# Optimization experiments

Hardware: AMD Instinct MI355X
Metric: run time of the kernel (lower is better)

The kernel has to match this reference:

```python
import jax, jax.numpy as jnp
import numpy as np

N_NODES = 100000   # n_users + n_items
N_EDGES = 1000000  # avg degree ~10
D = 64             # embed_dim
N_LAYERS = 3


def setup_inputs() -> dict:
    key = jax.random.key(0)
    k1, k2, k3, k4 = jax.random.split(key, 4)
    embedding = jax.random.normal(k1, (N_NODES, D), dtype=jnp.float32)
    src = jax.random.randint(k2, (N_EDGES,), 0, N_NODES)
    dst = jax.random.randint(k3, (N_EDGES,), 0, N_NODES)
    # sqrt_degree is a per-node [N,1] positive scale (1/sqrt(deg) in practice)
    sqrt_degree = jax.random.uniform(k4, (N_NODES, 1), dtype=jnp.float32,
                                     minval=0.01, maxval=1.0)
    return {"embedding": embedding, "sqrt_degree": sqrt_degree,
            "src": src, "dst": dst, "n_layers": N_LAYERS}


def reference(embedding, sqrt_degree, src, dst, n_layers):
    n_nodes = embedding.shape[0]
    h = embedding
    acc = embedding  # ego embedding (layer 0)
    for _ in range(n_layers):
        # Aggregator: scale, copy_src gather, segment-sum scatter, scale
        msg = (h * sqrt_degree)[src]                                   # [E, D]
        h = jax.ops.segment_sum(msg, dst, num_segments=n_nodes)        # [N, D]
        h = h * sqrt_degree
        acc = acc + h
    # torch.mean(torch.stack(all_embed, -1), -1)
    return acc / jnp.asarray(n_layers + 1, dtype=embedding.dtype)
```

## Files before the change

### kernel.cpp

```cpp
#include <hip/hip_runtime.h>
#include <hip/hip_fp16.h>


#define N_NODES 100000
#define D 64
#define ND4 (N_NODES * D / 4)
#define SCAN_B 1024
#define NTILES ((N_NODES + SCAN_B - 1) / SCAN_B)
#define NSLICE 8
#define SLICE_DIV 12500
#define D_MASK 0x1FFFF

typedef float        f4v __attribute__((ext_vector_type(4)));
typedef unsigned int u4v __attribute__((ext_vector_type(4)));

union H4 { uint2 u; __half2 h[2]; };
union H8 { u4v u; __half2 h[4]; };

__global__ void init_hist_kernel(const float4* __restrict__ emb,
                                 const float* __restrict__ deg,
                                 const int* __restrict__ dst,
                                 uint2* __restrict__ hs,
                                 int* __restrict__ cnt,
                                 unsigned int* __restrict__ key,
                                 int n4, int nedges) {
    int i = blockIdx.x * blockDim.x + threadIdx.x;
    if (i < nedges) {
        int d = dst[i];
        int r = atomicAdd(&cnt[d], 1);
        key[i] = (unsigned int)d | ((unsigned int)r << 17);
    }
    if (i >= n4) return;
    float dg = deg[i >> 4];
    float4 v = emb[i];
    H4 x;
    x.h[0] = __float22half2_rn(make_float2(v.x * dg, v.y * dg));
    x.h[1] = __float22half2_rn(make_float2(v.z * dg, v.w * dg));
    hs[i] = x.u;
}

__global__ void scanA_kernel(const int* __restrict__ cnt, int* __restrict__ off,
                             int* __restrict__ tsum, int n) {
    __shared__ int sm[SCAN_B];
    int t = threadIdx.x;
    int i = blockIdx.x * SCAN_B + t;
    int x = (i < n) ? cnt[i] : 0;
    sm[t] = x;
    __syncthreads();
    for (int o = 1; o < SCAN_B; o <<= 1) {
        int v = (t >= o) ? sm[t - o] : 0;
        __syncthreads();
        sm[t] += v;
        __syncthreads();
    }
    if (i < n) off[i] = sm[t] - x;
    if (t == SCAN_B - 1) tsum[blockIdx.x] = sm[t];
}

__global__ void scanB_kernel(int* __restrict__ tsum, int ntiles) {
    __shared__ int sm[SCAN_B];
    int t = threadIdx.x;
    int x = (t < ntiles) ? tsum[t] : 0;
    sm[t] = x;
    __syncthreads();
    for (int o = 1; o < SCAN_B; o <<= 1) {
        int v = (t >= o) ? sm[t - o] : 0;
        __syncthreads();
        sm[t] += v;
        __syncthreads();
    }
    if (t < ntiles) tsum[t] = sm[t] - x;
}

__global__ void scanC_kernel(int* __restrict__ off, const int* __restrict__ tsum,
                             int n, int nedges) {
    int i = blockIdx.x * blockDim.x + threadIdx.x;
    if (i >= n) return;
    off[i] += tsum[i >> 10];
    if (i == 0) off[n] = nedges;
}

__global__ void reorder_kernel(const int* __restrict__ src,
                               const unsigned int* __restrict__ key,
                               const int* __restrict__ off,
                               int* __restrict__ ssrc, int nedges) {
    int slice = blockIdx.x & (NSLICE - 1);
    int e = (blockIdx.x >> 3) * blockDim.x + threadIdx.x;
    if (e >= nedges) return;
    unsigned int k = __builtin_nontemporal_load(&key[e]);
    int d = (int)(k & D_MASK);
    if (d / SLICE_DIV != slice) return;
    int r = (int)(k >> 17);
    int p = off[d] + r;
    ssrc[p] = __builtin_nontemporal_load(&src[e]);
}

__device__ __forceinline__ void acc_h8(float* s, u4v u) {
    H8 x; x.u = u;
    #pragma unroll
    for (int k = 0; k < 4; ++k) {
        float2 f = __half22float2(x.h[k]);
        s[2 * k]     += f.x;
        s[2 * k + 1] += f.y;
    }
}

__global__ void aggregate_kernel(const u4v* __restrict__ hs_in,
                                 const int* __restrict__ off,
                                 const int* __restrict__ ssrc,
                                 const float* __restrict__ deg,
                                 const f4v* __restrict__ acc_in,
                                 f4v* __restrict__ acc_out,
                                 u4v* __restrict__ hs_out,
                                 int write_hs, float scale) {
    int tid = blockIdx.x * blockDim.x + threadIdx.x;
    int n = tid >> 3;
    if (n >= N_NODES) return;
    int d8 = tid & 7;
    int start = off[n];
    int end = off[n + 1];
    float s[8] = {0.f, 0.f, 0.f, 0.f, 0.f, 0.f, 0.f, 0.f};

    int j = start;
    for (; j + 8 <= end; j += 8) {
        int i0 = __builtin_nontemporal_load(&ssrc[j]);
        int i1 = __builtin_nontemporal_load(&ssrc[j + 1]);
        int i2 = __builtin_nontemporal_load(&ssrc[j + 2]);
        int i3 = __builtin_nontemporal_load(&ssrc[j + 3]);
        int i4 = __builtin_nontemporal_load(&ssrc[j + 4]);
        int i5 = __builtin_nontemporal_load(&ssrc[j + 5]);
        int i6 = __builtin_nontemporal_load(&ssrc[j + 6]);
        int i7 = __builtin_nontemporal_load(&ssrc[j + 7]);
        u4v v0 = hs_in[i0 * 8 + d8];
        u4v v1 = hs_in[i1 * 8 + d8];
        u4v v2 = hs_in[i2 * 8 + d8];
        u4v v3 = hs_in[i3 * 8 + d8];
        u4v v4 = hs_in[i4 * 8 + d8];
        u4v v5 = hs_in[i5 * 8 + d8];
        u4v v6 = hs_in[i6 * 8 + d8];
        u4v v7 = hs_in[i7 * 8 + d8];
        acc_h8(s, v0); acc_h8(s, v1); acc_h8(s, v2); acc_h8(s, v3);
        acc_h8(s, v4); acc_h8(s, v5); acc_h8(s, v6); acc_h8(s, v7);
    }
    for (; j + 4 <= end; j += 4) {
        int i0 = __builtin_nontemporal_load(&ssrc[j]);
        int i1 = __builtin_nontemporal_load(&ssrc[j + 1]);
        int i2 = __builtin_nontemporal_load(&ssrc[j + 2]);
        int i3 = __builtin_nontemporal_load(&ssrc[j + 3]);
        u4v v0 = hs_in[i0 * 8 + d8];
        u4v v1 = hs_in[i1 * 8 + d8];
        u4v v2 = hs_in[i2 * 8 + d8];
        u4v v3 = hs_in[i3 * 8 + d8];
        acc_h8(s, v0); acc_h8(s, v1); acc_h8(s, v2); acc_h8(s, v3);
    }
    for (; j < end; ++j) {
        acc_h8(s, hs_in[__builtin_nontemporal_load(&ssrc[j]) * 8 + d8]);
    }

    float dg = deg[n];
    float t[8];
    #pragma unroll
    for (int k = 0; k < 8; ++k) t[k] = s[k] * dg;

    int base = n * 16 + d8 * 2;
    f4v a0 = __builtin_nontemporal_load(&acc_in[base]);
    f4v a1 = __builtin_nontemporal_load(&acc_in[base + 1]);
    a0.x = (a0.x + t[0]) * scale;
    a0.y = (a0.y + t[1]) * scale;
    a0.z = (a0.z + t[2]) * scale;
    a0.w = (a0.w + t[3]) * scale;
    a1.x = (a1.x + t[4]) * scale;
    a1.y = (a1.y + t[5]) * scale;
    a1.z = (a1.z + t[6]) * scale;
    a1.w = (a1.w + t[7]) * scale;
    __builtin_nontemporal_store(a0, &acc_out[base]);
    __builtin_nontemporal_store(a1, &acc_out[base + 1]);

    if (write_hs) {
        H8 o;
        #pragma unroll
        for (int k = 0; k < 4; ++k)
            o.h[k] = __float22half2_rn(
                make_float2(t[2 * k] * dg, t[2 * k + 1] * dg));
        __builtin_nontemporal_store(o.u, &hs_out[tid]);
    }
}

extern "C" void kernel_launch(void* const* d_in, const int* in_sizes, int n_in,
                              void* d_out, int out_size, void* d_ws, size_t ws_size,
                              hipStream_t stream) {
    const float* emb = (const float*)d_in[0];
    const float* deg = (const float*)d_in[1];
    const int*   src = (const int*)d_in[2];
    const int*   dst = (const int*)d_in[3];
    float* out = (float*)d_out;
    int nedges = in_sizes[2];

    __half* hs_a = (__half*)d_ws;
    __half* hs_b = hs_a + (size_t)N_NODES * D;
    int*   ssrc   = (int*)(hs_b + (size_t)N_NODES * D);
    unsigned int* key = (unsigned int*)(ssrc + nedges);
    int*   cnt    = (int*)(key + nedges);
    int*   off    = cnt + N_NODES;
    int*   tsum   = off + N_NODES + 1;

    (void)hipMemsetAsync(cnt, 0, N_NODES * sizeof(int), stream);
    init_hist_kernel<<<(ND4 + 255) / 256, 256, 0, stream>>>(
        (const float4*)emb, deg, dst, (uint2*)hs_a, cnt, key, ND4, nedges);
    scanA_kernel<<<NTILES, SCAN_B, 0, stream>>>(cnt, off, tsum, N_NODES);
    scanB_kernel<<<1, SCAN_B, 0, stream>>>(tsum, NTILES);
    scanC_kernel<<<(N_NODES + 255) / 256, 256, 0, stream>>>(
        off, tsum, N_NODES, nedges);
    reorder_kernel<<<NSLICE * ((nedges + 255) / 256), 256, 0, stream>>>(
        src, key, off, ssrc, nedges);

    int nthreads = N_NODES * 8;
    int grid = (nthreads + 255) / 256;
    aggregate_kernel<<<grid, 256, 0, stream>>>(
        (const u4v*)hs_a, off, ssrc, deg, (const f4v*)emb,
        (f4v*)out, (u4v*)hs_b, 1, 1.0f);
    aggregate_kernel<<<grid, 256, 0, stream>>>(
        (const u4v*)hs_b, off, ssrc, deg, (const f4v*)out,
        (f4v*)out, (u4v*)hs_a, 1, 1.0f);
    aggregate_kernel<<<grid, 256, 0, stream>>>(
        (const u4v*)hs_a, off, ssrc, deg, (const f4v*)out,
        (f4v*)out, (u4v*)hs_b, 0, 0.25f);
}
```

Measured before the change: 251.5 us.

## Replace global-atomic CSR build with two-pass bucketed counting sort

The CSR construction no longer uses per-edge global atomics on a 100k-entry counter array followed by a three-kernel scan and an 8-slice reorder. It now builds a coarse bucket histogram per block in shared memory, scans it in a single block, scatters packed (src, local dst) words into buckets, and finishes with a per-bucket shared-memory counting sort that also writes the node offsets. This is meant to cut global atomic contention and scattered writes during preprocessing. In exchange it adds serial work in the one-block scan and final_kernel launches of only 98 large blocks. It also depends on hard-coded limits: 98 buckets of 1024 nodes, 128 edge blocks, and src indices that fit in 17 bits.

```diff
diff --git a/kernel.cpp b/kernel.cpp
--- a/kernel.cpp
+++ b/kernel.cpp
@@ -5,11 +5,11 @@
 #define N_NODES 100000
 #define D 64
 #define ND4 (N_NODES * D / 4)
-#define SCAN_B 1024
-#define NTILES ((N_NODES + SCAN_B - 1) / SCAN_B)
-#define NSLICE 8
-#define SLICE_DIV 12500
 #define D_MASK 0x1FFFF
+#define EPB 8192
+#define NBUCK 98
+#define BUCK_SHIFT 10
+#define NBLK_MAX 128
 
 typedef float        f4v __attribute__((ext_vector_type(4)));
 typedef unsigned int u4v __attribute__((ext_vector_type(4)));
@@ -17,19 +17,10 @@
 union H4 { uint2 u; __half2 h[2]; };
 union H8 { u4v u; __half2 h[4]; };
 
-__global__ void init_hist_kernel(const float4* __restrict__ emb,
-                                 const float* __restrict__ deg,
-                                 const int* __restrict__ dst,
-                                 uint2* __restrict__ hs,
-                                 int* __restrict__ cnt,
-                                 unsigned int* __restrict__ key,
-                                 int n4, int nedges) {
+__global__ void init_kernel(const float4* __restrict__ emb,
+                            const float* __restrict__ deg,
+                            uint2* __restrict__ hs, int n4) {
     int i = blockIdx.x * blockDim.x + threadIdx.x;
-    if (i < nedges) {
-        int d = dst[i];
-        int r = atomicAdd(&cnt[d], 1);
-        key[i] = (unsigned int)d | ((unsigned int)r << 17);
-    }
     if (i >= n4) return;
     float dg = deg[i >> 4];
     float4 v = emb[i];
@@ -39,60 +30,101 @@
     hs[i] = x.u;
 }
 
-__global__ void scanA_kernel(const int* __restrict__ cnt, int* __restrict__ off,
-                             int* __restrict__ tsum, int n) {
-    __shared__ int sm[SCAN_B];
-    int t = threadIdx.x;
-    int i = blockIdx.x * SCAN_B + t;
-    int x = (i < n) ? cnt[i] : 0;
-    sm[t] = x;
-    __syncthreads();
-    for (int o = 1; o < SCAN_B; o <<= 1) {
-        int v = (t >= o) ? sm[t - o] : 0;
-        __syncthreads();
-        sm[t] += v;
-        __syncthreads();
-    }
-    if (i < n) off[i] = sm[t] - x;
-    if (t == SCAN_B - 1) tsum[blockIdx.x] = sm[t];
-}
-
-__global__ void scanB_kernel(int* __restrict__ tsum, int ntiles) {
-    __shared__ int sm[SCAN_B];
-    int t = threadIdx.x;
-    int x = (t < ntiles) ? tsum[t] : 0;
-    sm[t] = x;
-    __syncthreads();
-    for (int o = 1; o < SCAN_B; o <<= 1) {
-        int v = (t >= o) ? sm[t - o] : 0;
-        __syncthreads();
-        sm[t] += v;
-        __syncthreads();
-    }
-    if (t < ntiles) tsum[t] = sm[t] - x;
-}
-
-__global__ void scanC_kernel(int* __restrict__ off, const int* __restrict__ tsum,
-                             int n, int nedges) {
-    int i = blockIdx.x * blockDim.x + threadIdx.x;
-    if (i >= n) return;
-    off[i] += tsum[i >> 10];
-    if (i == 0) off[n] = nedges;
-}
-
-__global__ void reorder_kernel(const int* __restrict__ src,
-                               const unsigned int* __restrict__ key,
-                               const int* __restrict__ off,
-                               int* __restrict__ ssrc, int nedges) {
-    int slice = blockIdx.x & (NSLICE - 1);
-    int e = (blockIdx.x >> 3) * blockDim.x + threadIdx.x;
-    if (e >= nedges) return;
-    unsigned int k = __builtin_nontemporal_load(&key[e]);
-    int d = (int)(k & D_MASK);
-    if (d / SLICE_DIV != slice) return;
-    int r = (int)(k >> 17);
-    int p = off[d] + r;
-    ssrc[p] = __builtin_nontemporal_load(&src[e]);
+__global__ void hist1_kernel(const int* __restrict__ dst,
+                             int* __restrict__ histg, int nedges, int nblk) {
+    __shared__ int hloc[NBUCK];
+    int t = threadIdx.x;
+    for (int i = t; i < NBUCK; i += 256) hloc[i] = 0;
+    __syncthreads();
+    int base = blockIdx.x * EPB;
+    int end = min(base + EPB, nedges);
+    for (int e = base + t; e < end; e += 256)
+        atomicAdd(&hloc[dst[e] >> BUCK_SHIFT], 1);
+    __syncthreads();
+    for (int i = t; i < NBUCK; i += 256)
+        histg[i * nblk + blockIdx.x] = hloc[i];
+}
+
+__global__ void scan_kernel(int* __restrict__ histg, int* __restrict__ off,
+                            int m, int nedges) {
+    __shared__ int part[1024];
+    int t = threadIdx.x;
+    int C = (m + 1023) / 1024;
+    int beg = t * C;
+    int fin = min(beg + C, m);
+    int s = 0;
+    for (int i = beg; i < fin; ++i) s += histg[i];
+    part[t] = s;
+    __syncthreads();
+    for (int o = 1; o < 1024; o <<= 1) {
+        int v = (t >= o) ? part[t - o] : 0;
+        __syncthreads();
+        part[t] += v;
+        __syncthreads();
+    }
+    int base = (t > 0) ? part[t - 1] : 0;
+    for (int i = beg; i < fin; ++i) {
+        int v = histg[i];
+        histg[i] = base;
+        base += v;
+    }
+    if (t == 0) off[N_NODES] = nedges;
+}
+
+__global__ void scatter1_kernel(const int* __restrict__ src,
+                                const int* __restrict__ dst,
+                                const int* __restrict__ histg,
+                                unsigned int* __restrict__ packed,
+                                int nedges, int nblk) {
+    __shared__ int cur[NBUCK];
+    int t = threadIdx.x;
+    for (int i = t; i < NBUCK; i += 256)
+        cur[i] = histg[i * nblk + blockIdx.x];
+    __syncthreads();
+    int base = blockIdx.x * EPB;
+    int end = min(base + EPB, nedges);
+    for (int e = base + t; e < end; e += 256) {
+        int d = dst[e];
+        int b = d >> BUCK_SHIFT;
+        int r = atomicAdd(&cur[b], 1);
+        packed[r] = (unsigned int)src[e] |
+                    ((unsigned int)(d & 1023) << 17);
+    }
+}
+
+__global__ void final_kernel(const unsigned int* __restrict__ packed,
+                             const int* __restrict__ histg,
+                             int* __restrict__ off, int* __restrict__ ssrc,
+                             int nedges, int nblk) {
+    __shared__ int cnt[1024];
+    int b = blockIdx.x;
+    int t = threadIdx.x;
+    int ebeg = histg[b * nblk];
+    int eend = (b + 1 < NBUCK) ? histg[(b + 1) * nblk] : nedges;
+    cnt[t] = 0;
+    __syncthreads();
+    for (int e = ebeg + t; e < eend; e += 1024)
+        atomicAdd(&cnt[packed[e] >> 17], 1);
+    __syncthreads();
+    int x = cnt[t];
+    for (int o = 1; o < 1024; o <<= 1) {
+        int v = (t >= o) ? cnt[t - o] : 0;
+        __syncthreads();
+        cnt[t] += v;
+        __syncthreads();
+    }
+    int excl = cnt[t] - x;
+    int node = (b << BUCK_SHIFT) + t;
+    if (node < N_NODES) off[node] = ebeg + excl;
+    __syncthreads();
+    cnt[t] = excl;
+    __syncthreads();
+    for (int e = ebeg + t; e < eend; e += 1024) {
+        unsigned int p = packed[e];
+        int dl = (int)(p >> 17);
+        int r = atomicAdd(&cnt[dl], 1);
+        ssrc[ebeg + r] = (int)(p & D_MASK);
+    }
 }
 
 __device__ __forceinline__ void acc_h8(float* s, u4v u) {
@@ -195,24 +227,23 @@
     const int*   dst = (const int*)d_in[3];
     float* out = (float*)d_out;
     int nedges = in_sizes[2];
+    int nblk = (nedges + EPB - 1) / EPB;
 
     __half* hs_a = (__half*)d_ws;
     __half* hs_b = hs_a + (size_t)N_NODES * D;
     int*   ssrc   = (int*)(hs_b + (size_t)N_NODES * D);
-    unsigned int* key = (unsigned int*)(ssrc + nedges);
-    int*   cnt    = (int*)(key + nedges);
-    int*   off    = cnt + N_NODES;
-    int*   tsum   = off + N_NODES + 1;
-
-    (void)hipMemsetAsync(cnt, 0, N_NODES * sizeof(int), stream);
-    init_hist_kernel<<<(ND4 + 255) / 256, 256, 0, stream>>>(
-        (const float4*)emb, deg, dst, (uint2*)hs_a, cnt, key, ND4, nedges);
-    scanA_kernel<<<NTILES, SCAN_B, 0, stream>>>(cnt, off, tsum, N_NODES);
-    scanB_kernel<<<1, SCAN_B, 0, stream>>>(tsum, NTILES);
-    scanC_kernel<<<(N_NODES + 255) / 256, 256, 0, stream>>>(
-        off, tsum, N_NODES, nedges);
-    reorder_kernel<<<NSLICE * ((nedges + 255) / 256), 256, 0, stream>>>(
-        src, key, off, ssrc, nedges);
+    unsigned int* packed = (unsigned int*)(ssrc + nedges);
+    int*   histg  = (int*)(packed + nedges);
+    int*   off    = histg + NBUCK * NBLK_MAX;
+
+    init_kernel<<<(ND4 + 255) / 256, 256, 0, stream>>>(
+        (const float4*)emb, deg, (uint2*)hs_a, ND4);
+    hist1_kernel<<<nblk, 256, 0, stream>>>(dst, histg, nedges, nblk);
+    scan_kernel<<<1, 1024, 0, stream>>>(histg, off, NBUCK * nblk, nedges);
+    scatter1_kernel<<<nblk, 256, 0, stream>>>(
+        src, dst, histg, packed, nedges, nblk);
+    final_kernel<<<NBUCK, 1024, 0, stream>>>(
+        packed, histg, off, ssrc, nedges, nblk);
 
     int nthreads = N_NODES * 8;
     int grid = (nthreads + 255) / 256;
```

Measured after the change: 242.3 us. 3.7% less time.
